# Optimization experiments

Measured on AMD Instinct MI355X. Metric: run time of the kernel, lower is better.

Reference implementation:

```python
import jax, jax.numpy as jnp
import numpy as np

TOP_K = 2

def setup_inputs() -> dict:
    key = jax.random.key(0)
    k1, k2, k3, k4 = jax.random.split(key, 4)
    B, S, D, E = 4, 4096, 2048, 8
    x = jax.random.normal(k1, (B, S, D), dtype=jnp.float32)
    w_g = jax.random.normal(k2, (E, D), dtype=jnp.float32) * (1.0 / np.sqrt(D))
    w_noise = jax.random.normal(k3, (E, D), dtype=jnp.float32) * (1.0 / np.sqrt(D))
    eps = jax.random.normal(k4, (B, S, E), dtype=jnp.float32)
    return {"x": x, "w_g": w_g, "w_noise": w_noise, "eps": eps}

def reference(x, w_g, w_noise, eps):
    # gate logits: [B, S, E]
    logits = jnp.einsum('bsd,ed->bse', x, w_g)
    # noisy top-k: logits += softplus(x @ w_noise.T) * eps
    noise = jax.nn.softplus(jnp.einsum('bsd,ed->bse', x, w_noise)) * eps
    logits = logits + noise
    top_k_logits, top_k_indices = jax.lax.top_k(logits, TOP_K)
    return (top_k_logits, top_k_indices)
```

## Files before the change

### kernel.cpp

```cpp
#include <hip/hip_runtime.h>
#include <math.h>

#define TOKENS 16384
#define DIM 2048
#define NE 8
#define BLOCK 1024
#define GRID 256
#define NCHUNK (DIM / 256)

__launch_bounds__(BLOCK, 4)
__global__ void router_kernel(const float* __restrict__ x,
                              const float* __restrict__ w_g,
                              const float* __restrict__ w_noise,
                              const float* __restrict__ eps,
                              float* __restrict__ out)
{
    __shared__ float wlds[16 * DIM];

    const int tid  = threadIdx.x;
    const int lane = tid & 63;
    const int wv   = tid >> 6;
    const int t0   = (blockIdx.x * 16 + wv) * 4;

    const float4* x4 = (const float4*)x;

    float4 xvA[4], xvB[4];
    #pragma unroll
    for (int t = 0; t < 4; ++t) xvA[t] = x4[(t0 + t) * (DIM / 4) + 0 * 64 + lane];
    #pragma unroll
    for (int t = 0; t < 4; ++t) xvB[t] = x4[(t0 + t) * (DIM / 4) + 1 * 64 + lane];

    float my_eps = 0.f;
    if (lane < 32) my_eps = eps[t0 * NE + lane];

    {
        const float4* g4 = (const float4*)w_g;
        const float4* n4 = (const float4*)w_noise;
        float4* l4 = (float4*)wlds;
        #pragma unroll
        for (int i = tid; i < (NE * DIM) / 4; i += BLOCK) {
            l4[i] = g4[i];
            l4[i + (NE * DIM) / 4] = n4[i];
        }
    }
    __syncthreads();

    const float4* wl4 = (const float4*)wlds;

    float V[64];
    #pragma unroll
    for (int v = 0; v < 64; ++v) V[v] = 0.f;

    #pragma unroll
    for (int kp = 0; kp < NCHUNK; kp += 2) {
        #pragma unroll
        for (int r = 0; r < 16; ++r) {
            const float4 w = wl4[r * (DIM / 4) + kp * 64 + lane];
            #pragma unroll
            for (int t = 0; t < 4; ++t) {
                float a = V[r * 4 + t];
                a = fmaf(xvA[t].x, w.x, a);
                a = fmaf(xvA[t].y, w.y, a);
                a = fmaf(xvA[t].z, w.z, a);
                a = fmaf(xvA[t].w, w.w, a);
                V[r * 4 + t] = a;
            }
        }
        if (kp + 2 < NCHUNK) {
            #pragma unroll
            for (int t = 0; t < 4; ++t)
                xvA[t] = x4[(t0 + t) * (DIM / 4) + (kp + 2) * 64 + lane];
        }
        #pragma unroll
        for (int r = 0; r < 16; ++r) {
            const float4 w = wl4[r * (DIM / 4) + (kp + 1) * 64 + lane];
            #pragma unroll
            for (int t = 0; t < 4; ++t) {
                float a = V[r * 4 + t];
                a = fmaf(xvB[t].x, w.x, a);
                a = fmaf(xvB[t].y, w.y, a);
                a = fmaf(xvB[t].z, w.z, a);
                a = fmaf(xvB[t].w, w.w, a);
                V[r * 4 + t] = a;
            }
        }
        if (kp + 3 < NCHUNK) {
            #pragma unroll
            for (int t = 0; t < 4; ++t)
                xvB[t] = x4[(t0 + t) * (DIM / 4) + (kp + 3) * 64 + lane];
        }
    }

    #pragma unroll
    for (int s = 0; s < 6; ++s) {
        const int m = 1 << s;
        const int n = 64 >> s;
        #pragma unroll
        for (int j = 0; j < n / 2; ++j) {
            const float A = V[2 * j];
            const float B = V[2 * j + 1];
            const float As = __shfl_xor(A, m, 64);
            const float Bs = __shfl_xor(B, m, 64);
            V[j] = (lane & m) ? (B + Bs) : (A + As);
        }
    }
    const float mine = V[0];

    const float other = __shfl_xor(mine, 32, 64);

    if (lane < 32) {
        const int e = lane >> 2;
        const int t = lane & 3;
        const int tok = t0 + t;

        const float ev = __shfl(my_eps, (t << 3) | e, 64);

        const float nv = other;
        const float sp = fmaxf(nv, 0.f) + log1pf(expf(-fabsf(nv)));
        const float logit = fmaf(sp, ev, mine);

        float v1 = logit, v2 = -INFINITY;
        int   i1 = e,     i2 = 7;
        #pragma unroll
        for (int sm = 2; sm <= 4; ++sm) {
            const int m = 1 << sm;
            const float ov1 = __shfl_xor(v1, m, 64);
            const float ov2 = __shfl_xor(v2, m, 64);
            const int   oi1 = __shfl_xor(i1, m, 64);
            const int   oi2 = __shfl_xor(i2, m, 64);
            const bool firstA = (v1 > ov1) || (v1 == ov1 && i1 < oi1);
            const float nv1 = firstA ? v1  : ov1;
            const int   ni1 = firstA ? i1  : oi1;
            const float ca  = firstA ? ov1 : v1;
            const int   cia = firstA ? oi1 : i1;
            const float cb  = firstA ? v2  : ov2;
            const int   cib = firstA ? i2  : oi2;
            const bool secondA = (ca > cb) || (ca == cb && cia < cib);
            v1 = nv1; i1 = ni1;
            v2 = secondA ? ca : cb;
            i2 = secondA ? cia : cib;
        }

        if (e == 0) {
            *(float2*)&out[2 * tok] = make_float2(v1, v2);
            *(float2*)&out[2 * TOKENS + 2 * tok] = make_float2((float)i1, (float)i2);
        }
    }
}

extern "C" void kernel_launch(void* const* d_in, const int* in_sizes, int n_in,
                              void* d_out, int out_size, void* d_ws, size_t ws_size,
                              hipStream_t stream) {
    const float* x       = (const float*)d_in[0];
    const float* w_g     = (const float*)d_in[1];
    const float* w_noise = (const float*)d_in[2];
    const float* eps     = (const float*)d_in[3];
    float* out = (float*)d_out;

    router_kernel<<<GRID, BLOCK, 0, stream>>>(x, w_g, w_noise, eps, out);
}
```

Before: 34.75 us.

## Stage weights via async global_load_lds in two halves and use DPP reductions

Weight staging into LDS now uses direct global-to-LDS loads, one row per wavefront, split into two halves. Compute on the first half of the K dimension starts after the first barrier while the second half is still loading. Each wavefront visits K chunks in a rotated order so concurrent waves read different LDS regions. The cross-lane butterfly reduction uses DPP moves for the xor-1, xor-2 and xor-8 steps instead of ds_bpermute shuffles, to cut LDS traffic and latency. The main risks are the correctness of the async-load ordering around the barriers (no explicit vmcnt wait is shown) and the DPP row-control encodings.

```diff
diff --git a/kernel.cpp b/kernel.cpp
--- a/kernel.cpp
+++ b/kernel.cpp
@@ -6,7 +6,47 @@
 #define NE 8
 #define BLOCK 1024
 #define GRID 256
-#define NCHUNK (DIM / 256)
+#define NCHUNK 8
+
+template <int CTRL>
+__device__ __forceinline__ float dpp_mov(float v) {
+    return __int_as_float(__builtin_amdgcn_update_dpp(
+        0, __float_as_int(v), CTRL, 0xf, 0xf, true));
+}
+#define DPP_XOR1 0xB1
+#define DPP_XOR2 0x4E
+#define DPP_XOR8 0x128
+
+__device__ __forceinline__ void stage16(const float* g, float* l) {
+    __builtin_amdgcn_global_load_lds(
+        (const __attribute__((address_space(1))) void*)g,
+        (__attribute__((address_space(3))) void*)l, 16, 0, 0);
+}
+
+#define FMA_BODY(XBUF, KC)                                         \
+    {                                                              \
+        const int kk = (KC);                                       \
+        _Pragma("unroll")                                          \
+        for (int r = 0; r < 16; ++r) {                             \
+            const float4 w = wl4[r * (DIM / 4) + kk * 64 + lane];  \
+            _Pragma("unroll")                                      \
+            for (int t = 0; t < 4; ++t) {                          \
+                float a = V[r * 4 + t];                            \
+                a = fmaf(XBUF[t].x, w.x, a);                       \
+                a = fmaf(XBUF[t].y, w.y, a);                       \
+                a = fmaf(XBUF[t].z, w.z, a);                       \
+                a = fmaf(XBUF[t].w, w.w, a);                       \
+                V[r * 4 + t] = a;                                  \
+            }                                                      \
+        }                                                          \
+    }
+#define REFILL(XBUF, KC)                                           \
+    {                                                              \
+        const int kk = (KC);                                       \
+        _Pragma("unroll")                                          \
+        for (int t = 0; t < 4; ++t)                                \
+            XBUF[t] = x4[(t0 + t) * (DIM / 4) + kk * 64 + lane];   \
+    }
 
 __launch_bounds__(BLOCK, 4)
 __global__ void router_kernel(const float* __restrict__ x,
@@ -21,88 +61,94 @@
     const int lane = tid & 63;
     const int wv   = tid >> 6;
     const int t0   = (blockIdx.x * 16 + wv) * 4;
+    const int off  = wv & 3;
+
+    int c[8];
+    #pragma unroll
+    for (int j = 0; j < 8; ++j)
+        c[j] = ((j + off) & 3) + ((j >= 4) ? 4 : 0);
+
+    const float* wrow = (wv < 8) ? (w_g + wv * DIM) : (w_noise + (wv - 8) * DIM);
+    float* lrow = &wlds[wv * DIM];
+
+    #pragma unroll
+    for (int i = 0; i < 4; ++i)
+        stage16(wrow + i * 256 + lane * 4, lrow + i * 256);
 
     const float4* x4 = (const float4*)x;
-
     float4 xvA[4], xvB[4];
     #pragma unroll
-    for (int t = 0; t < 4; ++t) xvA[t] = x4[(t0 + t) * (DIM / 4) + 0 * 64 + lane];
-    #pragma unroll
-    for (int t = 0; t < 4; ++t) xvB[t] = x4[(t0 + t) * (DIM / 4) + 1 * 64 + lane];
+    for (int t = 0; t < 4; ++t) xvA[t] = x4[(t0 + t) * (DIM / 4) + c[0] * 64 + lane];
+    #pragma unroll
+    for (int t = 0; t < 4; ++t) xvB[t] = x4[(t0 + t) * (DIM / 4) + c[1] * 64 + lane];
 
     float my_eps = 0.f;
     if (lane < 32) my_eps = eps[t0 * NE + lane];
 
+    __syncthreads();
+
+    #pragma unroll
+    for (int i = 0; i < 4; ++i)
+        stage16(wrow + 1024 + i * 256 + lane * 4, lrow + 1024 + i * 256);
+
+    const float4* wl4 = (const float4*)wlds;
+
+    float V[64];
+    #pragma unroll
+    for (int v = 0; v < 64; ++v) V[v] = 0.f;
+
+    FMA_BODY(xvA, c[0]); REFILL(xvA, c[2]);
+    FMA_BODY(xvB, c[1]); REFILL(xvB, c[3]);
+    FMA_BODY(xvA, c[2]); REFILL(xvA, c[4]);
+    FMA_BODY(xvB, c[3]); REFILL(xvB, c[5]);
+
+    __syncthreads();
+
+    FMA_BODY(xvA, c[4]); REFILL(xvA, c[6]);
+    FMA_BODY(xvB, c[5]); REFILL(xvB, c[7]);
+    FMA_BODY(xvA, c[6]);
+    FMA_BODY(xvB, c[7]);
+
+    #pragma unroll
+    for (int j = 0; j < 32; ++j) {
+        const float A = V[2 * j], B = V[2 * j + 1];
+        const float As = dpp_mov<DPP_XOR1>(A);
+        const float Bs = dpp_mov<DPP_XOR1>(B);
+        V[j] = (lane & 1) ? (B + Bs) : (A + As);
+    }
+    #pragma unroll
+    for (int j = 0; j < 16; ++j) {
+        const float A = V[2 * j], B = V[2 * j + 1];
+        const float As = dpp_mov<DPP_XOR2>(A);
+        const float Bs = dpp_mov<DPP_XOR2>(B);
+        V[j] = (lane & 2) ? (B + Bs) : (A + As);
+    }
+    #pragma unroll
+    for (int j = 0; j < 8; ++j) {
+        const float A = V[2 * j], B = V[2 * j + 1];
+        const float As = __shfl_xor(A, 4, 64);
+        const float Bs = __shfl_xor(B, 4, 64);
+        V[j] = (lane & 4) ? (B + Bs) : (A + As);
+    }
+    #pragma unroll
+    for (int j = 0; j < 4; ++j) {
+        const float A = V[2 * j], B = V[2 * j + 1];
+        const float As = dpp_mov<DPP_XOR8>(A);
+        const float Bs = dpp_mov<DPP_XOR8>(B);
+        V[j] = (lane & 8) ? (B + Bs) : (A + As);
+    }
+    #pragma unroll
+    for (int j = 0; j < 2; ++j) {
+        const float A = V[2 * j], B = V[2 * j + 1];
+        const float As = __shfl_xor(A, 16, 64);
+        const float Bs = __shfl_xor(B, 16, 64);
+        V[j] = (lane & 16) ? (B + Bs) : (A + As);
+    }
     {
-        const float4* g4 = (const float4*)w_g;
-        const float4* n4 = (const float4*)w_noise;
-        float4* l4 = (float4*)wlds;
-        #pragma unroll
-        for (int i = tid; i < (NE * DIM) / 4; i += BLOCK) {
-            l4[i] = g4[i];
-            l4[i + (NE * DIM) / 4] = n4[i];
-        }
-    }
-    __syncthreads();
-
-    const float4* wl4 = (const float4*)wlds;
-
-    float V[64];
-    #pragma unroll
-    for (int v = 0; v < 64; ++v) V[v] = 0.f;
-
-    #pragma unroll
-    for (int kp = 0; kp < NCHUNK; kp += 2) {
-        #pragma unroll
-        for (int r = 0; r < 16; ++r) {
-            const float4 w = wl4[r * (DIM / 4) + kp * 64 + lane];
-            #pragma unroll
-            for (int t = 0; t < 4; ++t) {
-                float a = V[r * 4 + t];
-                a = fmaf(xvA[t].x, w.x, a);
-                a = fmaf(xvA[t].y, w.y, a);
-                a = fmaf(xvA[t].z, w.z, a);
-                a = fmaf(xvA[t].w, w.w, a);
-                V[r * 4 + t] = a;
-            }
-        }
-        if (kp + 2 < NCHUNK) {
-            #pragma unroll
-            for (int t = 0; t < 4; ++t)
-                xvA[t] = x4[(t0 + t) * (DIM / 4) + (kp + 2) * 64 + lane];
-        }
-        #pragma unroll
-        for (int r = 0; r < 16; ++r) {
-            const float4 w = wl4[r * (DIM / 4) + (kp + 1) * 64 + lane];
-            #pragma unroll
-            for (int t = 0; t < 4; ++t) {
-                float a = V[r * 4 + t];
-                a = fmaf(xvB[t].x, w.x, a);
-                a = fmaf(xvB[t].y, w.y, a);
-                a = fmaf(xvB[t].z, w.z, a);
-                a = fmaf(xvB[t].w, w.w, a);
-                V[r * 4 + t] = a;
-            }
-        }
-        if (kp + 3 < NCHUNK) {
-            #pragma unroll
-            for (int t = 0; t < 4; ++t)
-                xvB[t] = x4[(t0 + t) * (DIM / 4) + (kp + 3) * 64 + lane];
-        }
-    }
-
-    #pragma unroll
-    for (int s = 0; s < 6; ++s) {
-        const int m = 1 << s;
-        const int n = 64 >> s;
-        #pragma unroll
-        for (int j = 0; j < n / 2; ++j) {
-            const float A = V[2 * j];
-            const float B = V[2 * j + 1];
-            const float As = __shfl_xor(A, m, 64);
-            const float Bs = __shfl_xor(B, m, 64);
-            V[j] = (lane & m) ? (B + Bs) : (A + As);
-        }
+        const float A = V[0], B = V[1];
+        const float As = __shfl_xor(A, 32, 64);
+        const float Bs = __shfl_xor(B, 32, 64);
+        V[0] = (lane & 32) ? (B + Bs) : (A + As);
     }
     const float mine = V[0];
 
```

New measurement: 32.27 us. -7.1%, faster.
